# Optimization experiments

Measured on AMD Instinct MI355X. Metric: run time of the kernel, lower is better.

## Reference

```python
import jax, jax.numpy as jnp
import numpy as np

VOCAB, DIM = 100000, 128
B, C, NEG = 4096, 20, 10


def _init_table(key):
    initrange = 0.5 / DIM
    w = jax.random.uniform(key, (VOCAB - 1, DIM), dtype=jnp.float32,
                           minval=-initrange, maxval=initrange)
    return jnp.concatenate([jnp.zeros((1, DIM), jnp.float32), w], axis=0)


def setup_inputs() -> dict:
    key = jax.random.key(0)
    k1, k2, k3, k4, k5 = jax.random.split(key, 5)
    i_words = jax.random.randint(k1, (1, B), 0, VOCAB)
    o_words = jax.random.randint(k2, (C, B), 0, VOCAB)
    n_words = jax.random.randint(k3, (B, C * NEG), 0, VOCAB)
    W_i = _init_table(k4)
    W_os = _init_table(k5)
    return {"i_words": i_words, "o_words": o_words, "n_words": n_words,
            "W_i": W_i, "W_os": W_os}


def reference(i_words, o_words, n_words, W_i, W_os):
    # permute to batch-major
    i_ctx = i_words.T[:, 0]          # [B]  (single center word per example)
    o_ctx = o_words.T                # [B, C]

    i_vec = W_i[i_ctx]               # [B, D]
    o_vec = W_os[o_ctx]              # [B, C, D]
    o_vec_n = -W_os[n_words]         # [B, C*NEG, D]

    # bmm(o_vec, i_vec^T).sum(-1) -> positive scores [B, C]
    pos = jnp.einsum('bcd,bd->bc', o_vec, i_vec)
    loss_pos = jax.nn.log_sigmoid(pos).mean(axis=-1)              # [B]

    # negative scores [B, C*NEG] -> [B, C, NEG] -> mean over NEG
    neg = jnp.einsum('bnd,bd->bn', o_vec_n, i_vec)
    loss_neg = jax.nn.log_sigmoid(neg).reshape(-1, C, NEG).mean(axis=-1)  # [B, C]

    loss = jnp.sum(loss_pos) + jnp.sum(loss_neg)
    return -loss
```

## Files before the change

kernel.cpp:

```cpp
#include <hip/hip_runtime.h>
#include <math.h>

#define VOCAB 100000
#define DIM 128
#define BATCH 4096
#define CTX 20
#define NEGS 10
#define NTARG 220
#define NB 32
#define ROWS_PER_B 3125
#define NGANG 256
#define CAPG 160
#define SPILL_MAX 8192
#define SPILL_BLOCKS 8

#define OFF_COUNTS   0u
#define OFF_SPILLCNT 8192u
#define OFF_SPILL    8320u
#define OFF_RECORDS  41088u
#define OFF_IVEC16   5283968u
#define OFF_WOS16    6332544u
#define WS_NEEDED    31932544u
#define CONV_BLOCKS  6250

#if defined(__has_builtin)
#if __has_builtin(__builtin_amdgcn_fdot2_f32_bf16)
#define USE_DOT2 1
#endif
#endif

#ifdef USE_DOT2
typedef __bf16 bf16x2_t __attribute__((ext_vector_type(2)));
__device__ __forceinline__ bf16x2_t u2bf2(unsigned u) {
    union { unsigned u; bf16x2_t v; } c; c.u = u; return c.v;
}
#endif

__device__ __forceinline__ float log_sigmoid_fast(float x) {
    float a = fabsf(x);
    return fminf(x, 0.0f) - __logf(1.0f + __expf(-a));
}

__device__ __forceinline__ unsigned short f2bf_rtne(float f) {
    unsigned u = __float_as_uint(f);
    return (unsigned short)((u + 0x7fffu + ((u >> 16) & 1u)) >> 16);
}
__device__ __forceinline__ unsigned packbf2(float lo, float hi) {
    return ((unsigned)f2bf_rtne(hi) << 16) | f2bf_rtne(lo);
}

__device__ __forceinline__ float dot16(uint4 a, uint4 b, uint4 va, uint4 vb) {
#ifdef USE_DOT2
    float pd;
    pd = __builtin_amdgcn_fdot2_f32_bf16(u2bf2(a.x), u2bf2(va.x), 0.0f, false);
    pd = __builtin_amdgcn_fdot2_f32_bf16(u2bf2(a.y), u2bf2(va.y), pd, false);
    pd = __builtin_amdgcn_fdot2_f32_bf16(u2bf2(a.z), u2bf2(va.z), pd, false);
    pd = __builtin_amdgcn_fdot2_f32_bf16(u2bf2(a.w), u2bf2(va.w), pd, false);
    pd = __builtin_amdgcn_fdot2_f32_bf16(u2bf2(b.x), u2bf2(vb.x), pd, false);
    pd = __builtin_amdgcn_fdot2_f32_bf16(u2bf2(b.y), u2bf2(vb.y), pd, false);
    pd = __builtin_amdgcn_fdot2_f32_bf16(u2bf2(b.z), u2bf2(vb.z), pd, false);
    pd = __builtin_amdgcn_fdot2_f32_bf16(u2bf2(b.w), u2bf2(vb.w), pd, false);
    return pd;
#else
    unsigned aw[8] = {a.x, a.y, a.z, a.w, b.x, b.y, b.z, b.w};
    unsigned vw[8] = {va.x, va.y, va.z, va.w, vb.x, vb.y, vb.z, vb.w};
    float pd = 0.0f;
    #pragma unroll
    for (int k = 0; k < 8; ++k) {
        pd = fmaf(__uint_as_float(aw[k] << 16),         __uint_as_float(vw[k] << 16),         pd);
        pd = fmaf(__uint_as_float(aw[k] & 0xffff0000u), __uint_as_float(vw[k] & 0xffff0000u), pd);
    }
    return pd;
#endif
}

__global__ __launch_bounds__(256) void prep_kernel(
    const int* __restrict__ i_words, const int* __restrict__ o_words,
    const int* __restrict__ n_words, const float4* __restrict__ W_i4,
    const float4* __restrict__ W_os4, unsigned* __restrict__ ivec16,
    unsigned short* __restrict__ wos16, unsigned* __restrict__ records,
    unsigned char* __restrict__ counts, unsigned* __restrict__ spillcnt,
    unsigned* __restrict__ spill)
{
    if (blockIdx.x >= 512) {
        unsigned tid2 = (blockIdx.x - 512) * 256 + threadIdx.x;
        float4 a = W_os4[tid2 * 2];
        float4 b = W_os4[tid2 * 2 + 1];
        ushort4 lo, hi;
        lo.x = f2bf_rtne(a.x); lo.y = f2bf_rtne(a.y);
        lo.z = f2bf_rtne(a.z); lo.w = f2bf_rtne(a.w);
        hi.x = f2bf_rtne(b.x); hi.y = f2bf_rtne(b.y);
        hi.z = f2bf_rtne(b.z); hi.w = f2bf_rtne(b.w);
        ((ushort4*)wos16)[tid2 * 2]     = lo;
        ((ushort4*)wos16)[tid2 * 2 + 1] = hi;
        return;
    }
    if (blockIdx.x >= 256) {
        int gtid = (blockIdx.x - 256) * 256 + threadIdx.x;
        int ex = gtid >> 4, part = gtid & 15;
        const float4* src = W_i4 + (size_t)i_words[ex] * 32 + part * 2;
        float4 a = src[0], b = src[1];
        uint4 w;
        w.x = packbf2(a.x, a.y); w.y = packbf2(a.z, a.w);
        w.z = packbf2(b.x, b.y); w.w = packbf2(b.z, b.w);
        ((uint4*)ivec16)[gtid] = w;
        return;
    }
    __shared__ unsigned lcnt[NB];
    __shared__ unsigned lrec[NB * CAPG];
    const int exl = threadIdx.x >> 4;
    const int tt  = threadIdx.x & 15;
    const int b   = blockIdx.x * 16 + exl;

    if (threadIdx.x < NB) lcnt[threadIdx.x] = 0;
    __syncthreads();

    for (int j = tt; j < NTARG; j += 16) {
        int idx; unsigned negbit;
        if (j < CTX) { idx = o_words[j * BATCH + b];                negbit = 0u; }
        else         { idx = n_words[b * (CTX * NEGS) + (j - CTX)]; negbit = 0x10000u; }
        unsigned bucket = (unsigned)idx / ROWS_PER_B;
        unsigned rl     = (unsigned)idx - bucket * ROWS_PER_B;
        unsigned slot = atomicAdd(&lcnt[bucket], 1u);
        if (slot < CAPG) {
            lrec[bucket * CAPG + slot] = rl | ((unsigned)exl << 12) | negbit;
        } else {
            unsigned s = atomicAdd(spillcnt, 1u);
            if (s < SPILL_MAX) spill[s] = ((unsigned)idx << 13) | ((unsigned)b << 1) | (negbit ? 1u : 0u);
        }
    }
    __syncthreads();
    if (threadIdx.x < NB) {
        unsigned c = lcnt[threadIdx.x];
        counts[threadIdx.x * NGANG + blockIdx.x] = (unsigned char)(c < CAPG ? c : CAPG);
    }
    for (int k = threadIdx.x; k < NB * CAPG; k += 256) {
        unsigned bucket = (unsigned)k / CAPG;
        unsigned within = (unsigned)k - bucket * CAPG;
        records[(bucket * NGANG + (unsigned)blockIdx.x) * CAPG + within] = lrec[k];
    }
}

__global__ __launch_bounds__(256) void bucket_loss_bf16_kernel(
    const unsigned short* __restrict__ wos16, const unsigned* __restrict__ ivec16,
    const float* __restrict__ W_os, const float* __restrict__ W_i,
    const int* __restrict__ i_words,
    const unsigned* __restrict__ records, const unsigned char* __restrict__ counts,
    const unsigned* __restrict__ spillcnt, const unsigned* __restrict__ spill,
    float* __restrict__ out)
{
    const int lane = threadIdx.x & 63;
    const int wv   = threadIdx.x >> 6;
    const int g    = lane >> 3;
    const int t    = lane & 7;
    float acc = 0.0f;
    const int lid = blockIdx.x;

    if (lid < 2048) {
        const int xcd  = lid & 7;
        const int q    = lid >> 3;
        const unsigned bucket = (unsigned)((xcd << 2) | (q >> 6));
        const unsigned gang   = (unsigned)(((q & 63) << 2) | wv);
        const unsigned cell   = bucket * NGANG + gang;
        const unsigned cnt    = counts[cell];
        const unsigned* rbase = records + cell * CAPG;
        const char* wosb = (const char*)wos16 + ((unsigned)t << 5);
        const char* ivb  = (const char*)ivec16 + ((gang << 12) + ((unsigned)t << 5));
        const unsigned rowbase = bucket * ROWS_PER_B;

        #pragma unroll 2
        for (unsigned j0 = 0; j0 < cnt; j0 += 8) {
            unsigned jg = j0 + (unsigned)g;
            unsigned jc = (jg < cnt) ? jg : (cnt - 1);
            unsigned rec = rbase[jc];
            unsigned rowg = rowbase + (rec & 0xfffu);
            const char* rp = wosb + (rowg << 8);
            uint4 r0 = *(const uint4*)rp;
            uint4 r1 = *(const uint4*)(rp + 16);
            const char* ip = ivb + (((rec >> 12) & 15u) << 8);
            uint4 v0 = *(const uint4*)ip;
            uint4 v1 = *(const uint4*)(ip + 16);
            float pd = dot16(r0, r1, v0, v1);
            pd += __shfl_xor(pd, 1);
            pd += __shfl_xor(pd, 2);
            pd += __shfl_xor(pd, 4);
            float term = (rec & 0x10000u)
                       ? (1.0f / NEGS) * log_sigmoid_fast(-pd)
                       : (1.0f / CTX)  * log_sigmoid_fast(pd);
            if (t == 0 && jg < cnt) acc += term;
        }
    } else {
        const int t16   = threadIdx.x & 15;
        const int grp16 = threadIdx.x >> 4;
        int sg = (lid - 2048) * 16 + grp16;
        unsigned ns = *spillcnt; if (ns > SPILL_MAX) ns = SPILL_MAX;
        for (unsigned s = sg; s < ns; s += 16 * SPILL_BLOCKS) {
            unsigned e = spill[s];
            unsigned row = e >> 13, bb = (e >> 1) & 4095u;
            const char* rp = (const char*)W_os + ((row << 9) + ((unsigned)t16 << 5));
            float4 r0 = *(const float4*)rp, r1 = *(const float4*)(rp + 16);
            const char* vp = (const char*)W_i + (((unsigned)i_words[bb] << 9) + ((unsigned)t16 << 5));
            float4 v0 = *(const float4*)vp, v1 = *(const float4*)(vp + 16);
            float pd = r0.x*v0.x + r0.y*v0.y + r0.z*v0.z + r0.w*v0.w
                     + r1.x*v1.x + r1.y*v1.y + r1.z*v1.z + r1.w*v1.w;
            pd += __shfl_xor(pd, 1);
            pd += __shfl_xor(pd, 2);
            pd += __shfl_xor(pd, 4);
            pd += __shfl_xor(pd, 8);
            float term = (e & 1u) ? (1.0f / NEGS) * log_sigmoid_fast(-pd)
                                  : (1.0f / CTX)  * log_sigmoid_fast(pd);
            if (t16 == 0) acc += term;
        }
    }

    acc += __shfl_xor(acc, 8);
    acc += __shfl_xor(acc, 16);
    acc += __shfl_xor(acc, 32);
    __shared__ float wsum[4];
    if (lane == 0) wsum[wv] = acc;
    __syncthreads();
    if (threadIdx.x == 0) {
        float sum = wsum[0] + wsum[1] + wsum[2] + wsum[3];
        if (sum != 0.0f) atomicAdd(out, -sum);
    }
}

__global__ __launch_bounds__(256) void sgns_loss_direct(
    const int* __restrict__ i_words, const int* __restrict__ o_words,
    const int* __restrict__ n_words, const float* __restrict__ W_i,
    const float* __restrict__ W_os, float* __restrict__ out)
{
    const int lane = threadIdx.x & 63;
    const int wave = threadIdx.x >> 6;
    const int w    = blockIdx.x * 4 + wave;
    const int b    = w >> 1;
    const int h    = w & 1;
    const int sub = lane >> 4;
    const int t   = lane & 15;
    const int j_begin = h ? 112 : 0;
    const int j_end   = h ? NTARG : 112;
    float acc = 0.0f;
    const int ic = i_words[b];
    const char* ibase = (const char*)W_i + (((unsigned)ic << 9) + ((unsigned)t << 5));
    float4 i0 = *(const float4*)(ibase);
    float4 i1 = *(const float4*)(ibase + 16);
    #pragma unroll 4
    for (int j0 = j_begin; j0 < j_end; j0 += 4) {
        int jj = j0 + sub;
        int idx; float sgn, wgt;
        if (jj < CTX) { idx = o_words[jj * BATCH + b]; sgn = 1.0f; wgt = 1.0f / CTX; }
        else { idx = n_words[b * (CTX * NEGS) + (jj - CTX)]; sgn = -1.0f; wgt = 1.0f / NEGS; }
        const char* obase = (const char*)W_os + (((unsigned)idx << 9) + ((unsigned)t << 5));
        float4 o0 = *(const float4*)(obase);
        float4 o1 = *(const float4*)(obase + 16);
        float p = i0.x*o0.x + i0.y*o0.y + i0.z*o0.z + i0.w*o0.w
                + i1.x*o1.x + i1.y*o1.y + i1.z*o1.z + i1.w*o1.w;
        p += __shfl_xor(p, 1); p += __shfl_xor(p, 2);
        p += __shfl_xor(p, 4); p += __shfl_xor(p, 8);
        acc += (t == 0) ? wgt * log_sigmoid_fast(sgn * p) : 0.0f;
    }
    acc += __shfl_xor(acc, 16);
    acc += __shfl_xor(acc, 32);
    __shared__ float ws[4];
    if (lane == 0) ws[wave] = acc;
    __syncthreads();
    if (threadIdx.x == 0) atomicAdd(out, -(ws[0] + ws[1] + ws[2] + ws[3]));
}

extern "C" void kernel_launch(void* const* d_in, const int* in_sizes, int n_in,
                              void* d_out, int out_size, void* d_ws, size_t ws_size,
                              hipStream_t stream) {
    const int*   i_words = (const int*)d_in[0];
    const int*   o_words = (const int*)d_in[1];
    const int*   n_words = (const int*)d_in[2];
    const float* W_i     = (const float*)d_in[3];
    const float* W_os    = (const float*)d_in[4];
    float* out = (float*)d_out;

    hipMemsetAsync(out, 0, sizeof(float), stream);

    if (ws_size < (size_t)WS_NEEDED) {
        sgns_loss_direct<<<2048, 256, 0, stream>>>(i_words, o_words, n_words, W_i, W_os, out);
        return;
    }

    char* ws = (char*)d_ws;
    unsigned char* counts   = (unsigned char*)(ws + OFF_COUNTS);
    unsigned*      spillcnt = (unsigned*)(ws + OFF_SPILLCNT);
    unsigned*      spill    = (unsigned*)(ws + OFF_SPILL);
    unsigned*      records  = (unsigned*)(ws + OFF_RECORDS);
    unsigned*      ivec16   = (unsigned*)(ws + OFF_IVEC16);
    unsigned short* wos16   = (unsigned short*)(ws + OFF_WOS16);

    hipMemsetAsync(spillcnt, 0, sizeof(unsigned), stream);

    prep_kernel<<<512 + CONV_BLOCKS, 256, 0, stream>>>(
        i_words, o_words, n_words, (const float4*)W_i, (const float4*)W_os,
        ivec16, wos16, records, counts, spillcnt, spill);
    bucket_loss_bf16_kernel<<<2048 + SPILL_BLOCKS, 256, 0, stream>>>(
        wos16, ivec16, W_os, W_i, i_words, records, counts, spillcnt, spill, out);
}
```

Measured before the change: 72.29 us.

## Split each gang cell across two waves and software-pipeline record and row loads

Each bucket/gang cell is now handled by two wavefronts that interleave 8-record chunks, which doubles the number of blocks in the bucket loss kernel. The loop is software-pipelined: the record index is fetched two iterations ahead and the bf16 table row one iteration ahead, so gather latency overlaps with the dot product and log-sigmoid. This targets latency-bound dependent gathers, at the cost of more blocks, more registers per thread and some redundant clamped loads at the tail.

After: 90.85 us. 1.26x slower.

```diff
diff --git a/kernel.cpp b/kernel.cpp
--- a/kernel.cpp
+++ b/kernel.cpp
@@ -156,11 +156,12 @@
     float acc = 0.0f;
     const int lid = blockIdx.x;
 
-    if (lid < 2048) {
+    if (lid < 4096) {
         const int xcd  = lid & 7;
         const int q    = lid >> 3;
-        const unsigned bucket = (unsigned)((xcd << 2) | (q >> 6));
-        const unsigned gang   = (unsigned)(((q & 63) << 2) | wv);
+        const unsigned bucket = (unsigned)((xcd << 2) | (q >> 7));
+        const unsigned gang   = (unsigned)(((q & 127) << 1) | (wv & 1));
+        const unsigned half   = (unsigned)(wv >> 1);
         const unsigned cell   = bucket * NGANG + gang;
         const unsigned cnt    = counts[cell];
         const unsigned* rbase = records + cell * CAPG;
@@ -168,31 +169,44 @@
         const char* ivb  = (const char*)ivec16 + ((gang << 12) + ((unsigned)t << 5));
         const unsigned rowbase = bucket * ROWS_PER_B;
 
-        #pragma unroll 2
-        for (unsigned j0 = 0; j0 < cnt; j0 += 8) {
-            unsigned jg = j0 + (unsigned)g;
-            unsigned jc = (jg < cnt) ? jg : (cnt - 1);
-            unsigned rec = rbase[jc];
-            unsigned rowg = rowbase + (rec & 0xfffu);
-            const char* rp = wosb + (rowg << 8);
-            uint4 r0 = *(const uint4*)rp;
-            uint4 r1 = *(const uint4*)(rp + 16);
-            const char* ip = ivb + (((rec >> 12) & 15u) << 8);
-            uint4 v0 = *(const uint4*)ip;
-            uint4 v1 = *(const uint4*)(ip + 16);
-            float pd = dot16(r0, r1, v0, v1);
-            pd += __shfl_xor(pd, 1);
-            pd += __shfl_xor(pd, 2);
-            pd += __shfl_xor(pd, 4);
-            float term = (rec & 0x10000u)
-                       ? (1.0f / NEGS) * log_sigmoid_fast(-pd)
-                       : (1.0f / CTX)  * log_sigmoid_fast(pd);
-            if (t == 0 && jg < cnt) acc += term;
+        if (cnt) {
+            unsigned j0 = half * 8;
+            unsigned jg0 = j0 + (unsigned)g;
+            unsigned jc0 = (jg0 < cnt) ? jg0 : cnt - 1;
+            unsigned recA = rbase[jc0];
+            const char* rpA = wosb + ((size_t)((rowbase + (recA & 0xfffu))) << 8);
+            uint4 r0A = *(const uint4*)rpA;
+            uint4 r1A = *(const uint4*)(rpA + 16);
+            unsigned jg1 = j0 + 16 + (unsigned)g;
+            unsigned jc1 = (jg1 < cnt) ? jg1 : cnt - 1;
+            unsigned recB = rbase[jc1];
+
+            for (; j0 < cnt; j0 += 16) {
+                unsigned jg = j0 + (unsigned)g;
+                const char* rpB = wosb + ((size_t)((rowbase + (recB & 0xfffu))) << 8);
+                uint4 r0B = *(const uint4*)rpB;
+                uint4 r1B = *(const uint4*)(rpB + 16);
+                unsigned jg2 = j0 + 32 + (unsigned)g;
+                unsigned jc2 = (jg2 < cnt) ? jg2 : cnt - 1;
+                unsigned recC = rbase[jc2];
+                const char* ip = ivb + (((recA >> 12) & 15u) << 8);
+                uint4 v0 = *(const uint4*)ip;
+                uint4 v1 = *(const uint4*)(ip + 16);
+                float pd = dot16(r0A, r1A, v0, v1);
+                pd += __shfl_xor(pd, 1);
+                pd += __shfl_xor(pd, 2);
+                pd += __shfl_xor(pd, 4);
+                float term = (recA & 0x10000u)
+                           ? (1.0f / NEGS) * log_sigmoid_fast(-pd)
+                           : (1.0f / CTX)  * log_sigmoid_fast(pd);
+                if (t == 0 && jg < cnt) acc += term;
+                recA = recB; recB = recC; r0A = r0B; r1A = r1B;
+            }
         }
     } else {
         const int t16   = threadIdx.x & 15;
         const int grp16 = threadIdx.x >> 4;
-        int sg = (lid - 2048) * 16 + grp16;
+        int sg = (lid - 4096) * 16 + grp16;
         unsigned ns = *spillcnt; if (ns > SPILL_MAX) ns = SPILL_MAX;
         for (unsigned s = sg; s < ns; s += 16 * SPILL_BLOCKS) {
             unsigned e = spill[s];
@@ -297,6 +311,6 @@
     prep_kernel<<<512 + CONV_BLOCKS, 256, 0, stream>>>(
         i_words, o_words, n_words, (const float4*)W_i, (const float4*)W_os,
         ivec16, wos16, records, counts, spillcnt, spill);
-    bucket_loss_bf16_kernel<<<2048 + SPILL_BLOCKS, 256, 0, stream>>>(
+    bucket_loss_bf16_kernel<<<4096 + SPILL_BLOCKS, 256, 0, stream>>>(
         wos16, ivec16, W_os, W_i, i_words, records, counts, spillcnt, spill, out);
 }
```
